# Performance work log

Measured on AMD Instinct MI355X. Metric: run time of the kernel, lower is better.

## Reference

```python
import jax, jax.numpy as jnp
import numpy as np

B, D, H = 1024, 1024, 4096  # batch, input_dim, hidden_dim
EPS = 1e-3  # keras LayerNormalization default epsilon


def layer_norm(x, gamma, beta):
    m = jnp.mean(x, axis=-1, keepdims=True)
    v = jnp.var(x, axis=-1, keepdims=True)
    return (x - m) * jax.lax.rsqrt(v + EPS) * gamma + beta


def setup_inputs() -> dict:
    key = jax.random.key(0)
    ks = jax.random.split(key, 8)
    C = D + H  # concat width for gate/FFN projections
    s_in = 0.02
    return {
        "x": jax.random.normal(ks[0], (B, D), jnp.float32),
        "hidden_state": jax.random.normal(ks[1], (B, H), jnp.float32),
        "W_u": jax.random.normal(ks[2], (C, H), jnp.float32) * s_in,
        "b_u": jnp.zeros((H,), jnp.float32),
        "W_r": jax.random.normal(ks[3], (C, H), jnp.float32) * s_in,
        "b_r": jnp.zeros((H,), jnp.float32),
        "W_g": jax.random.normal(ks[4], (C, H), jnp.float32) * s_in,
        "b_g": jnp.zeros((H,), jnp.float32),
        "W_up": jax.random.normal(ks[5], (C, H), jnp.float32) * s_in,
        "b_up": jnp.zeros((H,), jnp.float32),
        "W_d": jax.random.normal(ks[6], (H, D), jnp.float32) * s_in,
        "b_d": jnp.zeros((D,), jnp.float32),
        "gamma_h": jnp.ones((H,), jnp.float32),
        "beta_h": jnp.zeros((H,), jnp.float32),
        "gamma_o": jnp.ones((D,), jnp.float32),
        "beta_o": jnp.zeros((D,), jnp.float32),
    }


def reference(x, hidden_state, W_u, b_u, W_r, b_r, W_g, b_g, W_up, b_up,
              W_d, b_d, gamma_h, beta_h, gamma_o, beta_o):
    h = hidden_state
    combined = jnp.concatenate([x, h], axis=-1)          # [B, D+H]
    u = jax.nn.sigmoid(combined @ W_u + b_u)             # update gate [B, H]
    r = jax.nn.sigmoid(combined @ W_r + b_r)             # reset gate  [B, H]
    cand = jnp.concatenate([x, r * h], axis=-1)          # [B, D+H]
    gate = cand @ W_g + b_g
    up = cand @ W_up + b_up
    swiglu = jax.nn.silu(gate) * up                      # [B, H]
    new_h = layer_norm((1.0 - u) * h + u * swiglu + h, gamma_h, beta_h)
    out = layer_norm(new_h @ W_d + b_d, gamma_o, beta_o)  # [B, D]
    return out, new_h
```

## Files before the change

kernel.cpp:

```cpp
#include <hip/hip_runtime.h>
#include <hip/hip_bf16.h>
#include <math.h>


typedef unsigned short u16;
typedef unsigned int u32;
typedef __attribute__((ext_vector_type(8))) short short8;
typedef __attribute__((ext_vector_type(4))) float floatx4;

#define B_ROWS 1024
#define H_DIM 4096
#define D_DIM 1024
#define LDA_S 72

__device__ __forceinline__ float bf2f(u16 v) {
  u32 u = ((u32)v) << 16;
  return __builtin_bit_cast(float, u);
}
__device__ __forceinline__ u16 f2bf(float f) {
  u32 u = __builtin_bit_cast(u32, f);
  u32 r = (u + 0x7fffu + ((u >> 16) & 1u)) >> 16;
  return (u16)r;
}

template <int MODE>
__launch_bounds__(256)
__global__ void gemm_k(const float* __restrict__ Af0, const float* __restrict__ Af1,
                       const u16* __restrict__ Ab,
                       const float* __restrict__ Bg0, const float* __restrict__ Bg1,
                       const float* __restrict__ bias0, const float* __restrict__ bias1,
                       const float* __restrict__ hglob,
                       float* __restrict__ outF, u16* __restrict__ outB0,
                       u16* __restrict__ outB1) {
  constexpr int K_TOT = (MODE == 3) ? 4096 : 5120;
  constexpr int KT = K_TOT / 64;
  constexpr int LDB = (MODE == 3) ? 1024 : 4096;

  const int n0 = blockIdx.x * 128;
  const int m0 = blockIdx.y * 128;
  const bool second = (MODE != 3) && (n0 >= 4096);
  const float* __restrict__ Bg = second ? Bg1 : Bg0;
  const int ncol0 = second ? (n0 - 4096) : n0;

  __shared__ __align__(16) u16 As[128 * LDA_S];
  __shared__ __align__(16) u16 Bs[64 * 128];

  const int t = threadIdx.x;
  const int w = t >> 6;
  const int lane = t & 63;
  const int q = lane >> 4;
  const int i16 = lane & 15;
  const int wm = (w >> 1) * 64;
  const int wn = (w & 1) * 64;

  floatx4 acc[4][4] = {};

  for (int kt = 0; kt < KT; ++kt) {
    const int k0 = kt * 64;
    const bool a_is_bf16 = (MODE == 2) && (k0 >= 1024);
    if (a_is_bf16) {
      const u16* Ag = Ab;
      const int lda = 4096;
      const int krel = k0 - 1024;
#pragma unroll
      for (int c = 0; c < 4; ++c) {
        const int p = c * 256 + t;
        const int row = p >> 3;
        const int cp = p & 7;
        const uint4 v = *(const uint4*)(Ag + (size_t)(m0 + row) * lda + krel + cp * 8);
        *(uint4*)(&As[row * LDA_S + cp * 8]) = v;
      }
    } else {
      const float* Ag;
      int lda, krel;
      if (MODE == 3)      { Ag = Af0; lda = 4096; krel = k0; }
      else if (k0 < 1024) { Ag = Af0; lda = 1024; krel = k0; }
      else                { Ag = Af1; lda = 4096; krel = k0 - 1024; }
#pragma unroll
      for (int c = 0; c < 8; ++c) {
        const int p = c * 256 + t;
        const int row = p >> 4;
        const int cp = p & 15;
        const float4 v = *(const float4*)(Ag + (size_t)(m0 + row) * lda + krel + cp * 4);
        ushort4 o;
        o.x = f2bf(v.x); o.y = f2bf(v.y); o.z = f2bf(v.z); o.w = f2bf(v.w);
        *(ushort4*)(&As[row * LDA_S + cp * 4]) = o;
      }
    }
#pragma unroll
    for (int cc = 0; cc < 2; ++cc) {
      const int c = 2 * w + cc;
      const float* bp = Bg + (size_t)(k0 + c * 8) * LDB + ncol0;
#pragma unroll
      for (int hn = 0; hn < 2; ++hn) {
        const int n = lane + hn * 64;
        const float* src = bp + n;
        u32 p0 = (u32)f2bf(src[0 * LDB]) | ((u32)f2bf(src[1 * LDB]) << 16);
        u32 p1 = (u32)f2bf(src[2 * LDB]) | ((u32)f2bf(src[3 * LDB]) << 16);
        u32 p2 = (u32)f2bf(src[4 * LDB]) | ((u32)f2bf(src[5 * LDB]) << 16);
        u32 p3 = (u32)f2bf(src[6 * LDB]) | ((u32)f2bf(src[7 * LDB]) << 16);
        *(uint4*)(&Bs[(size_t)(c * 128 + n) * 8]) = make_uint4(p0, p1, p2, p3);
      }
    }
    __syncthreads();
#pragma unroll
    for (int s = 0; s < 2; ++s) {
      short8 av[4], bv[4];
#pragma unroll
      for (int tm = 0; tm < 4; ++tm) {
        const int r = wm + tm * 16 + i16;
        av[tm] = *(const short8*)(&As[r * LDA_S + (s * 4 + q) * 8]);
      }
#pragma unroll
      for (int tn = 0; tn < 4; ++tn) {
        const int n = wn + tn * 16 + i16;
        const int c = s * 4 + q;
        bv[tn] = *(const short8*)(&Bs[(size_t)(c * 128 + n) * 8]);
      }
#pragma unroll
      for (int tm = 0; tm < 4; ++tm)
#pragma unroll
        for (int tn = 0; tn < 4; ++tn)
          acc[tm][tn] = __builtin_amdgcn_mfma_f32_16x16x32_bf16(av[tm], bv[tn], acc[tm][tn], 0, 0, 0);
    }
    __syncthreads();
  }

  const float* __restrict__ biasP = second ? bias1 : bias0;
  constexpr int LDO = (MODE == 3) ? 1024 : 4096;
#pragma unroll
  for (int tm = 0; tm < 4; ++tm) {
#pragma unroll
    for (int tn = 0; tn < 4; ++tn) {
      const int nloc = ncol0 + wn + tn * 16 + i16;
      const float b = biasP[nloc];
      const int mbase = m0 + wm + tm * 16 + q * 4;
#pragma unroll
      for (int r = 0; r < 4; ++r) {
        const int m = mbase + r;
        const float v = acc[tm][tn][r] + b;
        const size_t oidx = (size_t)m * LDO + nloc;
        if (MODE == 1) {
          const float sg = 1.f / (1.f + __expf(-v));
          if (!second) outF[oidx] = sg;
          else         outB0[oidx] = f2bf(sg * hglob[oidx]);
        } else if (MODE == 2) {
          if (!second) outB0[oidx] = f2bf(v);
          else         outB1[oidx] = f2bf(v);
        } else {
          outF[oidx] = v;
        }
      }
    }
  }
}

__launch_bounds__(256)
__global__ void ln_h_k(const float* u_f, const u16* __restrict__ wsg,
                       const u16* __restrict__ wsup, const float* __restrict__ h,
                       const float* __restrict__ gamma, const float* __restrict__ beta,
                       float* out) {
  const int row = blockIdx.x, t = threadIdx.x;
  const size_t base = (size_t)row * H_DIM;
  const int i0 = t * 16;
  float tv[16];
  float s = 0.f, s2 = 0.f;
#pragma unroll
  for (int j = 0; j < 16; ++j) {
    const int idx = i0 + j;
    const float u = u_f[base + idx];
    const float g = bf2f(wsg[base + idx]);
    const float up = bf2f(wsup[base + idx]);
    const float hh = h[base + idx];
    const float sw = (g / (1.f + __expf(-g))) * up;
    const float x = (2.f - u) * hh + u * sw;
    tv[j] = x; s += x; s2 += x * x;
  }
#pragma unroll
  for (int off = 32; off; off >>= 1) {
    s += __shfl_down(s, off);
    s2 += __shfl_down(s2, off);
  }
  __shared__ float red[8];
  const int w = t >> 6, lane = t & 63;
  if (lane == 0) { red[w] = s; red[4 + w] = s2; }
  __syncthreads();
  const float S = red[0] + red[1] + red[2] + red[3];
  const float S2 = red[4] + red[5] + red[6] + red[7];
  const float mean = S * (1.f / (float)H_DIM);
  const float var = fmaxf(S2 * (1.f / (float)H_DIM) - mean * mean, 0.f);
  const float rstd = rsqrtf(var + 1e-3f);
#pragma unroll
  for (int j = 0; j < 16; ++j) {
    const int idx = i0 + j;
    out[base + idx] = (tv[j] - mean) * rstd * gamma[idx] + beta[idx];
  }
}

__launch_bounds__(256)
__global__ void ln_o_k(float* io, const float* __restrict__ gamma,
                       const float* __restrict__ beta) {
  const int row = blockIdx.x, t = threadIdx.x;
  const size_t base = (size_t)row * D_DIM;
  const int i0 = t * 4;
  float tv[4];
  float s = 0.f, s2 = 0.f;
#pragma unroll
  for (int j = 0; j < 4; ++j) {
    const float x = io[base + i0 + j];
    tv[j] = x; s += x; s2 += x * x;
  }
#pragma unroll
  for (int off = 32; off; off >>= 1) {
    s += __shfl_down(s, off);
    s2 += __shfl_down(s2, off);
  }
  __shared__ float red[8];
  const int w = t >> 6, lane = t & 63;
  if (lane == 0) { red[w] = s; red[4 + w] = s2; }
  __syncthreads();
  const float S = red[0] + red[1] + red[2] + red[3];
  const float S2 = red[4] + red[5] + red[6] + red[7];
  const float mean = S * (1.f / (float)D_DIM);
  const float var = fmaxf(S2 * (1.f / (float)D_DIM) - mean * mean, 0.f);
  const float rstd = rsqrtf(var + 1e-3f);
#pragma unroll
  for (int j = 0; j < 4; ++j) {
    const int idx = i0 + j;
    io[base + idx] = (tv[j] - mean) * rstd * gamma[idx] + beta[idx];
  }
}

extern "C" void kernel_launch(void* const* d_in, const int* in_sizes, int n_in,
                              void* d_out, int out_size, void* d_ws, size_t ws_size,
                              hipStream_t stream) {
  (void)in_sizes; (void)n_in; (void)out_size; (void)ws_size;
  const float* x       = (const float*)d_in[0];
  const float* h       = (const float*)d_in[1];
  const float* W_u     = (const float*)d_in[2];
  const float* b_u     = (const float*)d_in[3];
  const float* W_r     = (const float*)d_in[4];
  const float* b_r     = (const float*)d_in[5];
  const float* W_g     = (const float*)d_in[6];
  const float* b_g     = (const float*)d_in[7];
  const float* W_up    = (const float*)d_in[8];
  const float* b_up    = (const float*)d_in[9];
  const float* W_d     = (const float*)d_in[10];
  const float* b_d     = (const float*)d_in[11];
  const float* gamma_h = (const float*)d_in[12];
  const float* beta_h  = (const float*)d_in[13];
  const float* gamma_o = (const float*)d_in[14];
  const float* beta_o  = (const float*)d_in[15];

  float* out_final = (float*)d_out;
  float* out_newh  = (float*)d_out + (size_t)B_ROWS * D_DIM;

  char* ws = (char*)d_ws;
  u16* ws_rh = (u16*)(ws);
  u16* ws_g  = (u16*)(ws + (size_t)8 * 1024 * 1024);
  u16* ws_up = (u16*)(ws + (size_t)16 * 1024 * 1024);
  float* u_buf = out_newh;
  float* o_pre = out_final;

  dim3 blk(256);
  gemm_k<1><<<dim3(64, 8), blk, 0, stream>>>(x, h, nullptr, W_u, W_r, b_u, b_r, h,
                                             u_buf, ws_rh, nullptr);
  gemm_k<2><<<dim3(64, 8), blk, 0, stream>>>(x, nullptr, ws_rh, W_g, W_up, b_g, b_up,
                                             nullptr, nullptr, ws_g, ws_up);
  ln_h_k<<<dim3(B_ROWS), blk, 0, stream>>>(u_buf, ws_g, ws_up, h, gamma_h, beta_h, out_newh);
  gemm_k<3><<<dim3(8, 8), blk, 0, stream>>>(out_newh, nullptr, nullptr, W_d, nullptr,
                                            b_d, nullptr, nullptr, o_pre, nullptr, nullptr);
  ln_o_k<<<dim3(B_ROWS), blk, 0, stream>>>(o_pre, gamma_o, beta_o);
}
```

Before: 744.0 us.

## Pre-pack operands into bf16 tile images and load via global_load_lds

Adds conversion kernels that turn fp32 weights and activations into bf16 tile-contiguous images each call. A new GEMM loads those images straight into LDS with global_load_lds and runs bf16 MFMA. The GEMM epilogue and the hidden-state LayerNorm write r*h and new_h directly in the image layout. This is meant to cut per-tile conversion and uncoalesced staging work inside the GEMM main loop. In exchange it adds extra passes over about 20M weight elements per call and needs a larger workspace, falling back to the old path when the workspace is too small.

```diff
diff --git a/kernel.cpp b/kernel.cpp
--- a/kernel.cpp
+++ b/kernel.cpp
@@ -21,6 +21,173 @@
   u32 u = __builtin_bit_cast(u32, f);
   u32 r = (u + 0x7fffu + ((u >> 16) & 1u)) >> 16;
   return (u16)r;
+}
+__device__ __forceinline__ u32 pkbf(float lo, float hi) {
+  return (u32)f2bf(lo) | ((u32)f2bf(hi) << 16);
+}
+
+__device__ __forceinline__ void gload_lds16(const u16* g, u16* l) {
+  __builtin_amdgcn_global_load_lds(
+      (const __attribute__((address_space(1))) void*)g,
+      (__attribute__((address_space(3))) void*)l, 16, 0, 0);
+}
+
+
+__launch_bounds__(256)
+__global__ void conv_w_k(const float* __restrict__ W0, const float* __restrict__ W1,
+                         u16* __restrict__ img, int ldb, int KT, int nbHalf) {
+  const int nb = blockIdx.x;
+  const int kt = blockIdx.y;
+  const float* W = (nb < nbHalf) ? W0 : W1;
+  const int nbl = (nb < nbHalf) ? nb : (nb - nbHalf);
+  const float* src = W + (size_t)kt * 64 * ldb + (size_t)nbl * 128;
+  u16* dst = img + ((size_t)nb * KT + kt) * 8192;
+  const int t = threadIdx.x;
+  const int n = t & 127;
+  const int half = t >> 7;
+#pragma unroll
+  for (int pass = 0; pass < 4; ++pass) {
+    const int kc = half * 4 + pass;
+    const float* sp = src + (size_t)(kc * 8) * ldb + n;
+    uint4 o;
+    o.x = pkbf(sp[0],                 sp[(size_t)ldb]);
+    o.y = pkbf(sp[(size_t)2 * ldb],   sp[(size_t)3 * ldb]);
+    o.z = pkbf(sp[(size_t)4 * ldb],   sp[(size_t)5 * ldb]);
+    o.w = pkbf(sp[(size_t)6 * ldb],   sp[(size_t)7 * ldb]);
+    *(uint4*)(dst + (size_t)(kc * 128 + n) * 8) = o;
+  }
+}
+
+__launch_bounds__(256)
+__global__ void conv_xh_k(const float* __restrict__ x, const float* __restrict__ h,
+                          u16* __restrict__ imgX, u16* __restrict__ imgH) {
+  const int kt = blockIdx.x;
+  const int mb = blockIdx.y;
+  const float* src;
+  u16* dst;
+  int lda;
+  if (kt < 16) {
+    lda = 1024;
+    src = x + (size_t)mb * 128 * lda + (size_t)kt * 64;
+    dst = imgX + ((size_t)mb * 16 + kt) * 8192;
+  } else {
+    lda = 4096;
+    src = h + (size_t)mb * 128 * lda + (size_t)(kt - 16) * 64;
+    dst = imgH + ((size_t)mb * 64 + (kt - 16)) * 8192;
+  }
+  const int t = threadIdx.x;
+  const int j = t & 127;
+  const int half = t >> 7;
+  const float* sp = src + (size_t)j * lda + half * 32;
+#pragma unroll
+  for (int pass = 0; pass < 4; ++pass) {
+    const int kc = half * 4 + pass;
+    const float4 a = *(const float4*)(sp + pass * 8);
+    const float4 b = *(const float4*)(sp + pass * 8 + 4);
+    uint4 o;
+    o.x = pkbf(a.x, a.y);
+    o.y = pkbf(a.z, a.w);
+    o.z = pkbf(b.x, b.y);
+    o.w = pkbf(b.z, b.w);
+    *(uint4*)(dst + (size_t)(kc * 128 + j) * 8) = o;
+  }
+}
+
+template <int MODE>
+__launch_bounds__(256)
+__global__ void gemm_img(const u16* __restrict__ A0, const u16* __restrict__ A1,
+                         const u16* __restrict__ Bimg,
+                         const float* __restrict__ bias0, const float* __restrict__ bias1,
+                         const float* __restrict__ hglob,
+                         float* __restrict__ outF, u16* __restrict__ outB0,
+                         u16* __restrict__ outB1) {
+  constexpr int KT = (MODE == 3) ? 64 : 80;
+  constexpr int KSPLIT = (MODE == 3) ? 64 : 16;
+  constexpr int A1T = KT - KSPLIT;
+
+  const int bx = blockIdx.x;
+  const int by = blockIdx.y;
+  const int n0 = bx * 128;
+  const int m0 = by * 128;
+  const bool second = (MODE != 3) && (n0 >= 4096);
+  const int ncol0 = second ? (n0 - 4096) : n0;
+
+  __shared__ __align__(16) u16 As[8192];
+  __shared__ __align__(16) u16 Bs[8192];
+
+  const int t = threadIdx.x;
+  const int w = t >> 6;
+  const int lane = t & 63;
+  const int q = lane >> 4;
+  const int i16 = lane & 15;
+  const int wm = (w >> 1) * 64;
+  const int wn = (w & 1) * 64;
+
+  floatx4 acc[4][4] = {};
+
+  const u16* at = A0 + (size_t)by * KSPLIT * 8192;
+  const u16* at1 = A1 + (size_t)by * A1T * 8192;
+  const u16* btk = Bimg + (size_t)bx * KT * 8192;
+
+  for (int kt = 0; kt < KT; ++kt) {
+#pragma unroll
+    for (int i = 0; i < 4; ++i) {
+      const int ch = (i * 4 + w) * 512;
+      gload_lds16(at + ch + lane * 8, &As[ch]);
+      gload_lds16(btk + ch + lane * 8, &Bs[ch]);
+    }
+    __syncthreads();
+#pragma unroll
+    for (int s = 0; s < 2; ++s) {
+      const int c = s * 4 + q;
+      short8 av[4], bv[4];
+#pragma unroll
+      for (int tm = 0; tm < 4; ++tm)
+        av[tm] = *(const short8*)(&As[(size_t)(c * 128 + wm + tm * 16 + i16) * 8]);
+#pragma unroll
+      for (int tn = 0; tn < 4; ++tn)
+        bv[tn] = *(const short8*)(&Bs[(size_t)(c * 128 + wn + tn * 16 + i16) * 8]);
+#pragma unroll
+      for (int tm = 0; tm < 4; ++tm)
+#pragma unroll
+        for (int tn = 0; tn < 4; ++tn)
+          acc[tm][tn] = __builtin_amdgcn_mfma_f32_16x16x32_bf16(av[tm], bv[tn], acc[tm][tn], 0, 0, 0);
+    }
+    __syncthreads();
+    at = (kt == KSPLIT - 1) ? at1 : (at + 8192);
+    btk += 8192;
+  }
+
+  const float* __restrict__ biasP = second ? bias1 : bias0;
+#pragma unroll
+  for (int tm = 0; tm < 4; ++tm) {
+#pragma unroll
+    for (int tn = 0; tn < 4; ++tn) {
+      const int nloc = ncol0 + wn + tn * 16 + i16;
+      const float b = biasP[nloc];
+      const int mbase = m0 + wm + tm * 16 + q * 4;
+#pragma unroll
+      for (int r = 0; r < 4; ++r) {
+        const int m = mbase + r;
+        const float v = acc[tm][tn][r] + b;
+        if (MODE == 1) {
+          const float sg = 1.f / (1.f + __expf(-v));
+          if (!second) {
+            outF[(size_t)m * 4096 + nloc] = sg;
+          } else {
+            const float rh = sg * hglob[(size_t)m * 4096 + nloc];
+            const size_t tb = ((size_t)(m >> 7) * 64 + (nloc >> 6)) * 8192;
+            outB0[tb + (size_t)((((nloc >> 3) & 7) * 128) + (m & 127)) * 8 + (nloc & 7)] = f2bf(rh);
+          }
+        } else if (MODE == 2) {
+          if (!second) outB0[(size_t)m * 4096 + nloc] = f2bf(v);
+          else         outB1[(size_t)m * 4096 + nloc] = f2bf(v);
+        } else {
+          outF[(size_t)m * 1024 + nloc] = v;
+        }
+      }
+    }
+  }
 }
 
 template <int MODE>
@@ -159,7 +326,7 @@
 __global__ void ln_h_k(const float* u_f, const u16* __restrict__ wsg,
                        const u16* __restrict__ wsup, const float* __restrict__ h,
                        const float* __restrict__ gamma, const float* __restrict__ beta,
-                       float* out) {
+                       float* out, u16* __restrict__ imgNH) {
   const int row = blockIdx.x, t = threadIdx.x;
   const size_t base = (size_t)row * H_DIM;
   const int i0 = t * 16;
@@ -191,9 +358,24 @@
   const float var = fmaxf(S2 * (1.f / (float)H_DIM) - mean * mean, 0.f);
   const float rstd = rsqrtf(var + 1e-3f);
 #pragma unroll
-  for (int j = 0; j < 16; ++j) {
-    const int idx = i0 + j;
-    out[base + idx] = (tv[j] - mean) * rstd * gamma[idx] + beta[idx];
+  for (int cc = 0; cc < 2; ++cc) {
+    float o[8];
+#pragma unroll
+    for (int jj = 0; jj < 8; ++jj) {
+      const int idx = i0 + cc * 8 + jj;
+      o[jj] = (tv[cc * 8 + jj] - mean) * rstd * gamma[idx] + beta[idx];
+      out[base + idx] = o[jj];
+    }
+    if (imgNH) {
+      const int idx8 = i0 + cc * 8;
+      uint4 v;
+      v.x = pkbf(o[0], o[1]);
+      v.y = pkbf(o[2], o[3]);
+      v.z = pkbf(o[4], o[5]);
+      v.w = pkbf(o[6], o[7]);
+      *(uint4*)(&imgNH[((size_t)(row >> 7) * 64 + (idx8 >> 6)) * 8192 +
+                       (size_t)((((idx8 >> 3) & 7) * 128) + (row & 127)) * 8]) = v;
+    }
   }
 }
 
@@ -234,7 +416,7 @@
 extern "C" void kernel_launch(void* const* d_in, const int* in_sizes, int n_in,
                               void* d_out, int out_size, void* d_ws, size_t ws_size,
                               hipStream_t stream) {
-  (void)in_sizes; (void)n_in; (void)out_size; (void)ws_size;
+  (void)in_sizes; (void)n_in; (void)out_size;
   const float* x       = (const float*)d_in[0];
   const float* h       = (const float*)d_in[1];
   const float* W_u     = (const float*)d_in[2];
@@ -254,21 +436,56 @@
 
   float* out_final = (float*)d_out;
   float* out_newh  = (float*)d_out + (size_t)B_ROWS * D_DIM;
-
-  char* ws = (char*)d_ws;
-  u16* ws_rh = (u16*)(ws);
-  u16* ws_g  = (u16*)(ws + (size_t)8 * 1024 * 1024);
-  u16* ws_up = (u16*)(ws + (size_t)16 * 1024 * 1024);
   float* u_buf = out_newh;
   float* o_pre = out_final;
 
   dim3 blk(256);
-  gemm_k<1><<<dim3(64, 8), blk, 0, stream>>>(x, h, nullptr, W_u, W_r, b_u, b_r, h,
-                                             u_buf, ws_rh, nullptr);
-  gemm_k<2><<<dim3(64, 8), blk, 0, stream>>>(x, nullptr, ws_rh, W_g, W_up, b_g, b_up,
-                                             nullptr, nullptr, ws_g, ws_up);
-  ln_h_k<<<dim3(B_ROWS), blk, 0, stream>>>(u_buf, ws_g, ws_up, h, gamma_h, beta_h, out_newh);
-  gemm_k<3><<<dim3(8, 8), blk, 0, stream>>>(out_newh, nullptr, nullptr, W_d, nullptr,
-                                            b_d, nullptr, nullptr, o_pre, nullptr, nullptr);
-  ln_o_k<<<dim3(B_ROWS), blk, 0, stream>>>(o_pre, gamma_o, beta_o);
-}
+
+  const size_t SZ_W  = (size_t)64 * 80 * 16384;
+  const size_t SZ_X  = (size_t)8 * 16 * 16384;
+  const size_t SZ_H  = (size_t)8 * 64 * 16384;
+  const size_t SZ_RH = SZ_H;
+  const size_t SZ_G  = (size_t)B_ROWS * H_DIM * 2;
+  const size_t SZ_UP = SZ_G;
+  const size_t NEED  = SZ_W + SZ_X + SZ_H + SZ_RH + SZ_G + SZ_UP;
+
+  if (ws_size >= NEED) {
+    char* ws = (char*)d_ws;
+    u16* imgW  = (u16*)(ws);
+    u16* imgX  = (u16*)(ws + SZ_W);
+    u16* imgH  = (u16*)(ws + SZ_W + SZ_X);
+    u16* imgNH = imgH;
+    u16* imgRH = (u16*)(ws + SZ_W + SZ_X + SZ_H);
+    u16* ws_g  = (u16*)(ws + SZ_W + SZ_X + SZ_H + SZ_RH);
+    u16* ws_up = (u16*)(ws + SZ_W + SZ_X + SZ_H + SZ_RH + SZ_G);
+
+    conv_xh_k<<<dim3(80, 8), blk, 0, stream>>>(x, h, imgX, imgH);
+    conv_w_k<<<dim3(64, 80), blk, 0, stream>>>(W_u, W_r, imgW, 4096, 80, 32);
+    gemm_img<1><<<dim3(64, 8), blk, 0, stream>>>(imgX, imgH, imgW, b_u, b_r, h,
+                                                 u_buf, imgRH, nullptr);
+    conv_w_k<<<dim3(64, 80), blk, 0, stream>>>(W_g, W_up, imgW, 4096, 80, 32);
+    gemm_img<2><<<dim3(64, 8), blk, 0, stream>>>(imgX, imgRH, imgW, b_g, b_up, nullptr,
+                                                 nullptr, ws_g, ws_up);
+    ln_h_k<<<dim3(B_ROWS), blk, 0, stream>>>(u_buf, ws_g, ws_up, h, gamma_h, beta_h,
+                                             out_newh, imgNH);
+    conv_w_k<<<dim3(8, 64), blk, 0, stream>>>(W_d, nullptr, imgW, 1024, 64, 8);
+    gemm_img<3><<<dim3(8, 8), blk, 0, stream>>>(imgNH, imgNH, imgW, b_d, nullptr, nullptr,
+                                                o_pre, nullptr, nullptr);
+    ln_o_k<<<dim3(B_ROWS), blk, 0, stream>>>(o_pre, gamma_o, beta_o);
+  } else {
+    char* ws = (char*)d_ws;
+    u16* ws_rh = (u16*)(ws);
+    u16* ws_g  = (u16*)(ws + (size_t)8 * 1024 * 1024);
+    u16* ws_up = (u16*)(ws + (size_t)16 * 1024 * 1024);
+
+    gemm_k<1><<<dim3(64, 8), blk, 0, stream>>>(x, h, nullptr, W_u, W_r, b_u, b_r, h,
+                                               u_buf, ws_rh, nullptr);
+    gemm_k<2><<<dim3(64, 8), blk, 0, stream>>>(x, nullptr, ws_rh, W_g, W_up, b_g, b_up,
+                                               nullptr, nullptr, ws_g, ws_up);
+    ln_h_k<<<dim3(B_ROWS), blk, 0, stream>>>(u_buf, ws_g, ws_up, h, gamma_h, beta_h,
+                                             out_newh, nullptr);
+    gemm_k<3><<<dim3(8, 8), blk, 0, stream>>>(out_newh, nullptr, nullptr, W_d, nullptr,
+                                              b_d, nullptr, nullptr, o_pre, nullptr, nullptr);
+    ln_o_k<<<dim3(B_ROWS), blk, 0, stream>>>(o_pre, gamma_o, beta_o);
+  }
+}
```

Result: faster. 699.2 us (-6.0%).
